# Performance work log

Measured on AMD Instinct MI355X. Metric: run time of the kernel, lower is better.

## Reference

```python
import jax, jax.numpy as jnp
import numpy as np

B = 4096          # batch of samples
M = 128           # n_orbitals
F = 32            # n_fermions
H = 512           # hidden_units


def setup_inputs() -> dict:
    key = jax.random.key(0)
    kn, kphi, kw1, kb1, kw2, kb2 = jax.random.split(key, 6)
    # occupancy strings: exactly F ones among M orbitals per sample
    keys = jax.random.split(kn, B)
    occ_idx = jax.vmap(lambda k: jax.random.permutation(k, M)[:F])(keys)  # [B,F]
    n = jnp.zeros((B, M), jnp.float32).at[jnp.arange(B)[:, None], occ_idx].set(1.0)
    # parameters
    Phi = jax.random.normal(kphi, (F, M), jnp.float32) * 0.1
    W1 = jax.random.normal(kw1, (M, H), jnp.float32) / np.sqrt(M)
    b1 = jnp.zeros((H,), jnp.float32)
    W2 = jax.random.normal(kw2, (H, F * M), jnp.float32) / np.sqrt(H)
    b2 = jnp.zeros((F * M,), jnp.float32)
    return {"n": n, "Phi": Phi, "W1": W1, "b1": b1, "W2": W2, "b2": b2}


def reference(n, Phi, W1, b1, W2, b2):
    # backflow MLP: Dense -> tanh -> Dense, reshaped to (F, M) per sample
    h = jnp.tanh(n @ W1 + b1)                       # [B,H]
    bf = (h @ W2 + b2).reshape(-1, F, M)            # [B,F,M]
    kernel = Phi[None] + bf                         # [B,F,M]
    # occupied orbital columns; exactly F ones per row, top_k is stable so
    # indices come out in ascending order (same as jnp.where(n, size=F))
    idx = jax.lax.top_k(n, F)[1]                    # [B,F] int32
    phi = jnp.take_along_axis(kernel, idx[:, None, :], axis=2)  # [B,F,F]
    sign, logabs = jnp.linalg.slogdet(phi)
    return jnp.log(sign.astype(jnp.complex64)) + logabs.astype(jnp.complex64)  # [B] complex
```

## Files before the change

kernel.cpp:

```cpp
#include <hip/hip_runtime.h>
#include <hip/hip_bf16.h>
#include <math.h>

#define B_N 4096
#define M_N 128
#define F_N 32
#define H_N 512
#define NFM 4096

#define WAVE_SYNC() do { \
  asm volatile("s_waitcnt lgkmcnt(0)" ::: "memory"); \
  __builtin_amdgcn_sched_barrier(0); \
} while (0)

__global__ __launch_bounds__(256) void k1_idx_h(
    const float* __restrict__ n, const float* __restrict__ W1,
    const float* __restrict__ b1, float* __restrict__ h_ws,
    unsigned int* __restrict__ mask)
{
  __shared__ int s_idx[F_N];
  __shared__ int s_cnt0;
  const int b = blockIdx.x;
  const int t = threadIdx.x;

  bool p = false;
  int before = 0;
  if (t < 128) {
    float v = n[(size_t)b * M_N + t];
    p = v > 0.5f;
    unsigned long long m = __ballot(p);
    int lane = t & 63;
    before = __popcll(m & ((1ull << lane) - 1ull));
    if (lane == 0) {
      if (t < 64) { mask[b*4+0] = (unsigned)m; mask[b*4+1] = (unsigned)(m>>32); }
      else        { mask[b*4+2] = (unsigned)m; mask[b*4+3] = (unsigned)(m>>32); }
    }
    if (t < 64) {
      if (lane == 0) s_cnt0 = __popcll(m);
      if (p) s_idx[before] = t;
    }
  }
  __syncthreads();
  if (t >= 64 && t < 128 && p) s_idx[s_cnt0 + before] = t;
  __syncthreads();

  #pragma unroll
  for (int cc = 0; cc < 2; ++cc) {
    int c = t + cc * 256;
    float acc = 0.0f;
    #pragma unroll
    for (int j = 0; j < F_N; ++j)
      acc += W1[(size_t)s_idx[j] * H_N + c];
    acc += b1[c];
    h_ws[(size_t)b * H_N + c] = tanhf(acc);
  }
}

__global__ __launch_bounds__(256) void k_w2t(
    const float* __restrict__ W2, float* __restrict__ W2t)
{
  __shared__ float lds[32 * 132];
  const int k = blockIdx.x;
  const int t = threadIdx.x;

  #pragma unroll
  for (int i = 0; i < 4; ++i) {
    int m0 = i * 1024 + t * 4;
    float4 v = *(const float4*)&W2[(size_t)k * NFM + m0];
    int ig = m0 >> 7, c = m0 & 127;
    lds[ig * 132 + c + 0] = v.x;
    lds[ig * 132 + c + 1] = v.y;
    lds[ig * 132 + c + 2] = v.z;
    lds[ig * 132 + c + 3] = v.w;
  }
  __syncthreads();

  const int c  = t >> 1;
  const int ih = (t & 1) * 16;
  float* outp = W2t + (size_t)c * (H_N * F_N) + k * F_N + ih;
  #pragma unroll
  for (int i = 0; i < 4; ++i) {
    int ig = ih + i * 4;
    float4 v = make_float4(lds[(ig + 0) * 132 + c], lds[(ig + 1) * 132 + c],
                           lds[(ig + 2) * 132 + c], lds[(ig + 3) * 132 + c]);
    *(float4*)(outp + i * 4) = v;
  }
}

__global__ __launch_bounds__(256) void k_count(
    const unsigned int* __restrict__ mask, int* __restrict__ bcnt)
{
  const int c = blockIdx.x;
  const int t = threadIdx.x;
  const int word = c >> 5, bit = c & 31;
  int sum = 0;
  for (int b = t; b < B_N; b += 256)
    sum += (int)((mask[(size_t)b*4 + word] >> bit) & 1u);
  #pragma unroll
  for (int off = 32; off > 0; off >>= 1) sum += __shfl_down(sum, off);
  __shared__ int s_s[4];
  if ((t & 63) == 0) s_s[t >> 6] = sum;
  __syncthreads();
  if (t == 0) bcnt[c] = s_s[0] + s_s[1] + s_s[2] + s_s[3];
}

__global__ __launch_bounds__(256) void k_fill(
    const unsigned int* __restrict__ mask, const int* __restrict__ bcnt,
    int* __restrict__ boff, int* __restrict__ bent, int* __restrict__ loc)
{
  const int c = blockIdx.x;
  const int t = threadIdx.x;
  const int w = t >> 6, lane = t & 63;
  __shared__ int s_wcnt[4];
  __shared__ int s_run;
  __shared__ int s_off;

  if (t == 0) {
    int o = 0;
    for (int i = 0; i < c; ++i) o += bcnt[i];
    s_off = o; boff[c] = o; s_run = 0;
  }
  __syncthreads();
  const int off = s_off;
  const int word = c >> 5, bit = c & 31;

  for (int chunk = 0; chunk < B_N; chunk += 256) {
    const int b = chunk + t;
    unsigned m0 = mask[(size_t)b*4+0], m1 = mask[(size_t)b*4+1];
    unsigned m2 = mask[(size_t)b*4+2], m3 = mask[(size_t)b*4+3];
    unsigned wv = (word == 0) ? m0 : (word == 1) ? m1 : (word == 2) ? m2 : m3;
    bool p = (wv >> bit) & 1u;
    int j = __popc(wv & ((1u << bit) - 1u));
    if (word > 0) j += __popc(m0);
    if (word > 1) j += __popc(m1);
    if (word > 2) j += __popc(m2);

    unsigned long long bal = __ballot(p);
    int before = __popcll(bal & ((1ull << lane) - 1ull));
    if (lane == 0) s_wcnt[w] = __popcll(bal);
    __syncthreads();
    int wbase = s_run;
    for (int i = 0; i < w; ++i) wbase += s_wcnt[i];
    if (p) {
      int pos = wbase + before;
      bent[(size_t)c * B_N + pos] = (b << 5) | j;
      loc[b * 32 + j] = off + pos;
    }
    __syncthreads();
    if (t == 0) s_run += s_wcnt[0] + s_wcnt[1] + s_wcnt[2] + s_wcnt[3];
    __syncthreads();
  }
}

__global__ __launch_bounds__(256) void k2_gemm_gather(
    const float* __restrict__ h, const float* __restrict__ W2t,
    const float* __restrict__ b2, const float* __restrict__ Phi,
    const int* __restrict__ bcnt, const int* __restrict__ boff,
    const int* __restrict__ bent, float* __restrict__ phi_bucket)
{
  __shared__ __align__(16) float smem[2 * 2624];
  __shared__ int s_b[128];

  const int tid = threadIdx.x;
  const int c   = blockIdx.x;
  const int cnt = bcnt[c];
  const int t0  = blockIdx.y * 128;
  if (t0 >= cnt) return;
  const int base = boff[c];
  const float* w2tc = W2t + (size_t)c * (H_N * F_N);

  if (tid < 128) {
    int ii = t0 + tid;
    int e  = bent[(size_t)c * B_N + (ii < cnt ? ii : cnt - 1)];
    s_b[tid] = e >> 5;
  }
  __syncthreads();

  const int kA  = tid & 15;
  const int rbA = (tid >> 4) * 8;
  const int tx  = tid & 7;
  const int tyr = tid >> 3;

  int rowb[8];
  #pragma unroll
  for (int i = 0; i < 8; ++i) rowb[i] = s_b[rbA + i];

  float acc[4][4];
  #pragma unroll
  for (int i = 0; i < 4; ++i)
    #pragma unroll
    for (int u = 0; u < 4; ++u) acc[i][u] = 0.f;

  float aReg[8], bReg0, bReg1;

  #pragma unroll
  for (int i = 0; i < 8; ++i)
    aReg[i] = h[(size_t)rowb[i] * H_N + kA];
  bReg0 = w2tc[tid];
  bReg1 = w2tc[256 + tid];
  *(float4*)&smem[kA * 132 + rbA] =
      make_float4(aReg[0], aReg[1], aReg[2], aReg[3]);
  *(float4*)&smem[kA * 132 + rbA + 4] =
      make_float4(aReg[4], aReg[5], aReg[6], aReg[7]);
  smem[2112 + tid] = bReg0;
  smem[2112 + 256 + tid] = bReg1;
  __syncthreads();

  #pragma unroll 1
  for (int t = 0; t < 32; ++t) {
    float* Atc = smem + (t & 1) * 2624;
    float* Btc = Atc + 2112;
    float* Atn = smem + ((t + 1) & 1) * 2624;
    float* Btn = Atn + 2112;

    if (t < 31) {
      int k0n = (t + 1) * 16;
      #pragma unroll
      for (int i = 0; i < 8; ++i)
        aReg[i] = h[(size_t)rowb[i] * H_N + k0n + kA];
      bReg0 = w2tc[k0n * 32 + tid];
      bReg1 = w2tc[k0n * 32 + 256 + tid];
    }

    #pragma unroll
    for (int kk = 0; kk < 16; ++kk) {
      float4 av = *(const float4*)&Atc[kk * 132 + tyr * 4];
      float4 bv = *(const float4*)&Btc[kk * 32 + tx * 4];
      float a4[4] = {av.x, av.y, av.z, av.w};
      float b4[4] = {bv.x, bv.y, bv.z, bv.w};
      #pragma unroll
      for (int i = 0; i < 4; ++i)
        #pragma unroll
        for (int u = 0; u < 4; ++u)
          acc[i][u] = fmaf(a4[i], b4[u], acc[i][u]);
    }

    if (t < 31) {
      *(float4*)&Atn[kA * 132 + rbA] =
          make_float4(aReg[0], aReg[1], aReg[2], aReg[3]);
      *(float4*)&Atn[kA * 132 + rbA + 4] =
          make_float4(aReg[4], aReg[5], aReg[6], aReg[7]);
      Btn[tid] = bReg0;
      Btn[256 + tid] = bReg1;
      __syncthreads();
    }
  }

  #pragma unroll
  for (int i = 0; i < 4; ++i) {
    int r = tyr * 4 + i;
    if (t0 + r < cnt) {
      int col = base + t0 + r;
      float v[4];
      #pragma unroll
      for (int u = 0; u < 4; ++u) {
        int ig   = tx * 4 + u;
        int colw = ig * M_N + c;
        v[u] = Phi[colw] + (acc[i][u] + b2[colw]);
      }
      *(float4*)&phi_bucket[(size_t)col * 32 + tx * 4] =
          make_float4(v[0], v[1], v[2], v[3]);
    }
  }
}

__global__ __launch_bounds__(256) void k3_det(
    const float* __restrict__ phi_bucket, const int* __restrict__ loc,
    float* __restrict__ out)
{
  __shared__ float A[4][32 * 33];
  const int w = threadIdx.x >> 6;
  const int lane = threadIdx.x & 63;
  const int b = blockIdx.x * 4 + w;
  float* Aw = A[w];

  {
    const int jj = lane & 31;
    const int hi = lane >> 5;
    int lcol = loc[b * 32 + jj];
    const float* colp = phi_bucket + (size_t)lcol * 32 + hi * 16;
    #pragma unroll
    for (int i = 0; i < 4; ++i) {
      float4 v = *(const float4*)(colp + i * 4);
      int ig = hi * 16 + i * 4;
      Aw[(ig + 0) * 33 + jj] = v.x;
      Aw[(ig + 1) * 33 + jj] = v.y;
      Aw[(ig + 2) * 33 + jj] = v.z;
      Aw[(ig + 3) * 33 + jj] = v.w;
    }
  }
  WAVE_SYNC();

  float logabs = 0.f;
  int negs = 0;
  for (int k = 0; k < 32; ++k) {
    float v = -1.f;
    int vi = lane;
    if (lane >= k && lane < 32) v = fabsf(Aw[lane * 33 + k]);
    #pragma unroll
    for (int off = 32; off > 0; off >>= 1) {
      float ov = __shfl_xor(v, off);
      int oi = __shfl_xor(vi, off);
      if (ov > v || (ov == v && oi < vi)) { v = ov; vi = oi; }
    }
    int p = vi;
    if (p != k) {
      negs ^= 1;
      if (lane < 32) {
        float tmp = Aw[k * 33 + lane];
        Aw[k * 33 + lane] = Aw[p * 33 + lane];
        Aw[p * 33 + lane] = tmp;
      }
    }
    WAVE_SYNC();
    float piv = Aw[k * 33 + k];
    if (piv < 0.f) negs ^= 1;
    logabs += logf(fabsf(piv));
    if (lane > k && lane < 32) {
      float l = Aw[lane * 33 + k];
      if (fabsf(piv) >= 1.17549435e-38f) l = l * (1.0f / piv);
      else                               l = l / piv;
      Aw[lane * 33 + k] = l;
    }
    WAVE_SYNC();
    if (lane > k && lane < 32) {
      int j = lane;
      float nukj = -Aw[k * 33 + j];
      for (int i = k + 1; i < 32; ++i)
        Aw[i * 33 + j] = fmaf(nukj, Aw[i * 33 + k], Aw[i * 33 + j]);
    }
    WAVE_SYNC();
  }

  if (lane == 0) {
    out[b]       = logabs;
    out[B_N + b] = (negs & 1) ? 3.14159265358979f : 0.0f;
  }
}

extern "C" void kernel_launch(void* const* d_in, const int* in_sizes, int n_in,
                              void* d_out, int out_size, void* d_ws, size_t ws_size,
                              hipStream_t stream) {
  const float* n   = (const float*)d_in[0];
  const float* Phi = (const float*)d_in[1];
  const float* W1  = (const float*)d_in[2];
  const float* b1  = (const float*)d_in[3];
  const float* W2  = (const float*)d_in[4];
  const float* b2  = (const float*)d_in[5];
  float* out = (float*)d_out;

  char* ws = (char*)d_ws;
  float*        h_ws       = (float*)ws;
  float*        phi_bucket = (float*)(ws + (size_t)8  * 1024 * 1024);
  float*        W2t        = (float*)(ws + (size_t)24 * 1024 * 1024);
  unsigned int* mask       = (unsigned int*)(ws + (size_t)32 * 1024 * 1024);
  int*          bent       = (int*)(ws + (size_t)32 * 1024 * 1024 + 65536);
  int*          loc        = (int*)(ws + (size_t)34 * 1024 * 1024 + 65536);
  int*          bcnt       = (int*)(ws + (size_t)34 * 1024 * 1024 + 65536 + 524288);
  int*          boff       = (int*)(ws + (size_t)34 * 1024 * 1024 + 65536 + 524288 + 4096);

  hipLaunchKernelGGL(k_w2t, dim3(H_N), dim3(256), 0, stream, W2, W2t);
  hipLaunchKernelGGL(k1_idx_h, dim3(B_N), dim3(256), 0, stream,
                     n, W1, b1, h_ws, mask);
  hipLaunchKernelGGL(k_count, dim3(M_N), dim3(256), 0, stream, mask, bcnt);
  hipLaunchKernelGGL(k_fill, dim3(M_N), dim3(256), 0, stream,
                     mask, bcnt, boff, bent, loc);
  hipLaunchKernelGGL(k2_gemm_gather, dim3(M_N, 32), dim3(256), 0, stream,
                     h_ws, W2t, b2, Phi, bcnt, boff, bent, phi_bucket);
  hipLaunchKernelGGL(k3_det, dim3(B_N / 4), dim3(256), 0, stream,
                     phi_bucket, loc, out);
}
```

Measured before the change: 198.6 us.

## Fuse count into fill, enlarge gather-GEMM tile, split det update across wave halves

```diff
diff --git a/kernel.cpp b/kernel.cpp
--- a/kernel.cpp
+++ b/kernel.cpp
@@ -87,42 +87,42 @@
   }
 }
 
-__global__ __launch_bounds__(256) void k_count(
-    const unsigned int* __restrict__ mask, int* __restrict__ bcnt)
-{
-  const int c = blockIdx.x;
-  const int t = threadIdx.x;
-  const int word = c >> 5, bit = c & 31;
-  int sum = 0;
-  for (int b = t; b < B_N; b += 256)
-    sum += (int)((mask[(size_t)b*4 + word] >> bit) & 1u);
-  #pragma unroll
-  for (int off = 32; off > 0; off >>= 1) sum += __shfl_down(sum, off);
-  __shared__ int s_s[4];
-  if ((t & 63) == 0) s_s[t >> 6] = sum;
-  __syncthreads();
-  if (t == 0) bcnt[c] = s_s[0] + s_s[1] + s_s[2] + s_s[3];
-}
-
 __global__ __launch_bounds__(256) void k_fill(
-    const unsigned int* __restrict__ mask, const int* __restrict__ bcnt,
-    int* __restrict__ boff, int* __restrict__ bent, int* __restrict__ loc)
+    const unsigned int* __restrict__ mask,
+    int* __restrict__ bcnt, int* __restrict__ boff,
+    int* __restrict__ bent, int* __restrict__ loc)
 {
   const int c = blockIdx.x;
   const int t = threadIdx.x;
   const int w = t >> 6, lane = t & 63;
+  const int word = c >> 5, bit = c & 31;
   __shared__ int s_wcnt[4];
+  __shared__ int s_red[8];
   __shared__ int s_run;
-  __shared__ int s_off;
-
-  if (t == 0) {
-    int o = 0;
-    for (int i = 0; i < c; ++i) o += bcnt[i];
-    s_off = o; boff[c] = o; s_run = 0;
-  }
-  __syncthreads();
-  const int off = s_off;
-  const int word = c >> 5, bit = c & 31;
+
+  int cnt_loc = 0, off_loc = 0;
+  for (int b = t; b < B_N; b += 256) {
+    unsigned m0 = mask[(size_t)b*4+0], m1 = mask[(size_t)b*4+1];
+    unsigned m2 = mask[(size_t)b*4+2], m3 = mask[(size_t)b*4+3];
+    unsigned wv = (word == 0) ? m0 : (word == 1) ? m1 : (word == 2) ? m2 : m3;
+    cnt_loc += (int)((wv >> bit) & 1u);
+    int r = __popc(wv & ((1u << bit) - 1u));
+    if (word > 0) r += __popc(m0);
+    if (word > 1) r += __popc(m1);
+    if (word > 2) r += __popc(m2);
+    off_loc += r;
+  }
+  #pragma unroll
+  for (int off = 32; off > 0; off >>= 1) {
+    cnt_loc += __shfl_down(cnt_loc, off);
+    off_loc += __shfl_down(off_loc, off);
+  }
+  if (lane == 0) { s_red[w] = cnt_loc; s_red[4 + w] = off_loc; }
+  __syncthreads();
+  const int cnt_tot = s_red[0] + s_red[1] + s_red[2] + s_red[3];
+  const int off_tot = s_red[4] + s_red[5] + s_red[6] + s_red[7];
+  if (t == 0) { bcnt[c] = cnt_tot; boff[c] = off_tot; s_run = 0; }
+  __syncthreads();
 
   for (int chunk = 0; chunk < B_N; chunk += 256) {
     const int b = chunk + t;
@@ -144,7 +144,7 @@
     if (p) {
       int pos = wbase + before;
       bent[(size_t)c * B_N + pos] = (b << 5) | j;
-      loc[b * 32 + j] = off + pos;
+      loc[b * 32 + j] = off_tot + pos;
     }
     __syncthreads();
     if (t == 0) s_run += s_wcnt[0] + s_wcnt[1] + s_wcnt[2] + s_wcnt[3];
@@ -158,18 +158,18 @@
     const int* __restrict__ bcnt, const int* __restrict__ boff,
     const int* __restrict__ bent, float* __restrict__ phi_bucket)
 {
-  __shared__ __align__(16) float smem[2 * 2624];
-  __shared__ int s_b[128];
+  __shared__ __align__(16) float smem[2 * 4672];
+  __shared__ int s_b[256];
 
   const int tid = threadIdx.x;
   const int c   = blockIdx.x;
   const int cnt = bcnt[c];
-  const int t0  = blockIdx.y * 128;
+  const int t0  = blockIdx.y * 256;
   if (t0 >= cnt) return;
   const int base = boff[c];
   const float* w2tc = W2t + (size_t)c * (H_N * F_N);
 
-  if (tid < 128) {
+  {
     int ii = t0 + tid;
     int e  = bent[(size_t)c * B_N + (ii < cnt ? ii : cnt - 1)];
     s_b[tid] = e >> 5;
@@ -177,46 +177,46 @@
   __syncthreads();
 
   const int kA  = tid & 15;
-  const int rbA = (tid >> 4) * 8;
+  const int rgA = tid >> 4;
   const int tx  = tid & 7;
   const int tyr = tid >> 3;
 
-  int rowb[8];
-  #pragma unroll
-  for (int i = 0; i < 8; ++i) rowb[i] = s_b[rbA + i];
-
-  float acc[4][4];
-  #pragma unroll
-  for (int i = 0; i < 4; ++i)
+  int rowb[16];
+  #pragma unroll
+  for (int i = 0; i < 16; ++i) rowb[i] = s_b[rgA * 16 + i];
+
+  float acc[8][4];
+  #pragma unroll
+  for (int i = 0; i < 8; ++i)
     #pragma unroll
     for (int u = 0; u < 4; ++u) acc[i][u] = 0.f;
 
-  float aReg[8], bReg0, bReg1;
-
-  #pragma unroll
-  for (int i = 0; i < 8; ++i)
+  float aReg[16], bReg0, bReg1;
+
+  #pragma unroll
+  for (int i = 0; i < 16; ++i)
     aReg[i] = h[(size_t)rowb[i] * H_N + kA];
   bReg0 = w2tc[tid];
   bReg1 = w2tc[256 + tid];
-  *(float4*)&smem[kA * 132 + rbA] =
-      make_float4(aReg[0], aReg[1], aReg[2], aReg[3]);
-  *(float4*)&smem[kA * 132 + rbA + 4] =
-      make_float4(aReg[4], aReg[5], aReg[6], aReg[7]);
-  smem[2112 + tid] = bReg0;
-  smem[2112 + 256 + tid] = bReg1;
+  #pragma unroll
+  for (int u = 0; u < 4; ++u)
+    *(float4*)&smem[kA * 260 + rgA * 16 + u * 4] =
+        make_float4(aReg[4*u], aReg[4*u+1], aReg[4*u+2], aReg[4*u+3]);
+  smem[4160 + tid] = bReg0;
+  smem[4160 + 256 + tid] = bReg1;
   __syncthreads();
 
   #pragma unroll 1
   for (int t = 0; t < 32; ++t) {
-    float* Atc = smem + (t & 1) * 2624;
-    float* Btc = Atc + 2112;
-    float* Atn = smem + ((t + 1) & 1) * 2624;
-    float* Btn = Atn + 2112;
+    float* Atc = smem + (t & 1) * 4672;
+    float* Btc = Atc + 4160;
+    float* Atn = smem + ((t + 1) & 1) * 4672;
+    float* Btn = Atn + 4160;
 
     if (t < 31) {
       int k0n = (t + 1) * 16;
       #pragma unroll
-      for (int i = 0; i < 8; ++i)
+      for (int i = 0; i < 16; ++i)
         aReg[i] = h[(size_t)rowb[i] * H_N + k0n + kA];
       bReg0 = w2tc[k0n * 32 + tid];
       bReg1 = w2tc[k0n * 32 + 256 + tid];
@@ -224,42 +224,47 @@
 
     #pragma unroll
     for (int kk = 0; kk < 16; ++kk) {
-      float4 av = *(const float4*)&Atc[kk * 132 + tyr * 4];
+      float4 a0 = *(const float4*)&Atc[kk * 260 + tyr * 8];
+      float4 a1 = *(const float4*)&Atc[kk * 260 + tyr * 8 + 4];
       float4 bv = *(const float4*)&Btc[kk * 32 + tx * 4];
-      float a4[4] = {av.x, av.y, av.z, av.w};
+      float a8[8] = {a0.x, a0.y, a0.z, a0.w, a1.x, a1.y, a1.z, a1.w};
       float b4[4] = {bv.x, bv.y, bv.z, bv.w};
       #pragma unroll
-      for (int i = 0; i < 4; ++i)
+      for (int i = 0; i < 8; ++i)
         #pragma unroll
         for (int u = 0; u < 4; ++u)
-          acc[i][u] = fmaf(a4[i], b4[u], acc[i][u]);
+          acc[i][u] = fmaf(a8[i], b4[u], acc[i][u]);
     }
 
     if (t < 31) {
-      *(float4*)&Atn[kA * 132 + rbA] =
-          make_float4(aReg[0], aReg[1], aReg[2], aReg[3]);
-      *(float4*)&Atn[kA * 132 + rbA + 4] =
-          make_float4(aReg[4], aReg[5], aReg[6], aReg[7]);
+      #pragma unroll
+      for (int u = 0; u < 4; ++u)
+        *(float4*)&Atn[kA * 260 + rgA * 16 + u * 4] =
+            make_float4(aReg[4*u], aReg[4*u+1], aReg[4*u+2], aReg[4*u+3]);
       Btn[tid] = bReg0;
       Btn[256 + tid] = bReg1;
       __syncthreads();
     }
   }
 
-  #pragma unroll
-  for (int i = 0; i < 4; ++i) {
-    int r = tyr * 4 + i;
+  float ph[4], bb[4];
+  #pragma unroll
+  for (int u = 0; u < 4; ++u) {
+    int colw = (tx * 4 + u) * M_N + c;
+    ph[u] = Phi[colw];
+    bb[u] = b2[colw];
+  }
+  #pragma unroll
+  for (int i = 0; i < 8; ++i) {
+    int r = tyr * 8 + i;
     if (t0 + r < cnt) {
       int col = base + t0 + r;
-      float v[4];
-      #pragma unroll
-      for (int u = 0; u < 4; ++u) {
-        int ig   = tx * 4 + u;
-        int colw = ig * M_N + c;
-        v[u] = Phi[colw] + (acc[i][u] + b2[colw]);
-      }
+      float v0 = ph[0] + (acc[i][0] + bb[0]);
+      float v1 = ph[1] + (acc[i][1] + bb[1]);
+      float v2 = ph[2] + (acc[i][2] + bb[2]);
+      float v3 = ph[3] + (acc[i][3] + bb[3]);
       *(float4*)&phi_bucket[(size_t)col * 32 + tx * 4] =
-          make_float4(v[0], v[1], v[2], v[3]);
+          make_float4(v0, v1, v2, v3);
     }
   }
 }
@@ -323,11 +328,16 @@
       Aw[lane * 33 + k] = l;
     }
     WAVE_SYNC();
-    if (lane > k && lane < 32) {
-      int j = lane;
-      float nukj = -Aw[k * 33 + j];
-      for (int i = k + 1; i < 32; ++i)
-        Aw[i * 33 + j] = fmaf(nukj, Aw[i * 33 + k], Aw[i * 33 + j]);
+    {
+      const int mid = (k + 33) >> 1;
+      const int j   = lane & 31;
+      const int ilo = (lane < 32) ? (k + 1) : mid;
+      const int ihi = (lane < 32) ? mid : 32;
+      if (j > k) {
+        float nukj = -Aw[k * 33 + j];
+        for (int i = ilo; i < ihi; ++i)
+          Aw[i * 33 + j] = fmaf(nukj, Aw[i * 33 + k], Aw[i * 33 + j]);
+      }
     }
     WAVE_SYNC();
   }
@@ -362,10 +372,9 @@
   hipLaunchKernelGGL(k_w2t, dim3(H_N), dim3(256), 0, stream, W2, W2t);
   hipLaunchKernelGGL(k1_idx_h, dim3(B_N), dim3(256), 0, stream,
                      n, W1, b1, h_ws, mask);
-  hipLaunchKernelGGL(k_count, dim3(M_N), dim3(256), 0, stream, mask, bcnt);
   hipLaunchKernelGGL(k_fill, dim3(M_N), dim3(256), 0, stream,
                      mask, bcnt, boff, bent, loc);
-  hipLaunchKernelGGL(k2_gemm_gather, dim3(M_N, 32), dim3(256), 0, stream,
+  hipLaunchKernelGGL(k2_gemm_gather, dim3(M_N, 16), dim3(256), 0, stream,
                      h_ws, W2t, b2, Phi, bcnt, boff, bent, phi_bucket);
   hipLaunchKernelGGL(k3_det, dim3(B_N / 4), dim3(256), 0, stream,
                      phi_bucket, loc, out);
```

Measured after the change: 225.2 us. 13.4% more time.
